# Kernel tuning notes

Measured on AMD Instinct MI355X. Metric: run time of the kernel, lower is better.

The kernel has to match this reference:

```python
import jax, jax.numpy as jnp
import numpy as np

B, IN_F, OUT_F, KD = 256, 1024, 128, 16


def setup_inputs() -> dict:
    key = jax.random.key(0)
    k1, k2 = jax.random.split(key)
    x = jax.random.normal(k1, (B, IN_F), dtype=jnp.float32)
    t_mat = jax.random.normal(k2, (IN_F, OUT_F, KD), dtype=jnp.float32)
    return {"x": x, "t_mat": t_mat}


def reference(x, t_mat):
    # Projection: [B, in] @ [in, out*kd] -> [B, out, kd]
    m = jnp.einsum('bi,iok->bok', x, t_mat)
    # All-pairs L1 distance over kernel dim: [B, B, out]
    norm = jnp.sum(jnp.abs(m[:, None, :, :] - m[None, :, :, :]), axis=-1)
    # exp(-norm) summed over the partner axis; subtract 1 for self-pair (norm=0 -> exp=1)
    o_b = jnp.sum(jnp.exp(-norm), axis=1) - 1.0  # [B, out]
    return jnp.concatenate([x, o_b], axis=1)  # [B, in + out]
```

## Files before the change

### kernel.cpp

```cpp
#include <hip/hip_runtime.h>
#include <hip/hip_fp16.h>


#define BATCH 256
#define INF   1024
#define OUTF  128
#define KDIM  16
#define TCOLS 2048
#define OCOLS 1152
#define XB    1032

typedef __attribute__((ext_vector_type(8))) short short8;
typedef __attribute__((ext_vector_type(4))) float f32x4;

__device__ inline unsigned pack_bf2(float lo, float hi) {
    return __builtin_amdgcn_perm(__float_as_uint(hi), __float_as_uint(lo), 0x07060302u);
}
__device__ inline unsigned short bf_trunc(float f) {
    return (unsigned short)(__float_as_uint(f) >> 16);
}

__global__ __launch_bounds__(256, 2) void k_gemm(const float* __restrict__ x,
                                                 const float* __restrict__ T,
                                                 __half* __restrict__ mh) {
    const int blk = blockIdx.x;
    const int o   = blk & 127;
    const int mq  = blk >> 7;
    const int tid = threadIdx.x;
    const int wave = tid >> 6, lane = tid & 63;
    const int l15 = lane & 15, q = lane >> 4;

    __shared__ unsigned short bs[16][XB];
    __shared__ __half pmout[64][16];

    {
        const int kb = tid >> 2, n0 = (tid & 3) * 4;
        #pragma unroll
        for (int pass = 0; pass < 16; ++pass) {
            const int k = pass * 64 + kb;
            float4 v = *reinterpret_cast<const float4*>(&T[k * TCOLS + o * KDIM + n0]);
            bs[n0 + 0][k] = bf_trunc(v.x);
            bs[n0 + 1][k] = bf_trunc(v.y);
            bs[n0 + 2][k] = bf_trunc(v.z);
            bs[n0 + 3][k] = bf_trunc(v.w);
        }
    }
    __syncthreads();

    const int mt = mq * 4 + wave;
    const float* xr = &x[(mt * 16 + l15) * INF + q * 8];

    float4 st[4][2];
    #pragma unroll
    for (int p = 0; p < 4; ++p) {
        st[p][0] = *reinterpret_cast<const float4*>(xr + p * 32);
        st[p][1] = *reinterpret_cast<const float4*>(xr + p * 32 + 4);
    }
    f32x4 acc = {0.f, 0.f, 0.f, 0.f};
    #pragma unroll
    for (int ks = 0; ks < 32; ++ks) {
        const int p = ks & 3;
        float4 a0 = st[p][0], a1 = st[p][1];
        const int kn = (ks + 4 < 32) ? ks + 4 : ks;
        st[p][0] = *reinterpret_cast<const float4*>(xr + kn * 32);
        st[p][1] = *reinterpret_cast<const float4*>(xr + kn * 32 + 4);
        short8 bfr = *reinterpret_cast<const short8*>(&bs[l15][ks * 32 + q * 8]);
        union { unsigned u[4]; short8 s; } ua;
        ua.u[0] = pack_bf2(a0.x, a0.y); ua.u[1] = pack_bf2(a0.z, a0.w);
        ua.u[2] = pack_bf2(a1.x, a1.y); ua.u[3] = pack_bf2(a1.z, a1.w);
        acc = __builtin_amdgcn_mfma_f32_16x16x32_bf16(ua.s, bfr, acc, 0, 0, 0);
    }

    #pragma unroll
    for (int r = 0; r < 4; ++r)
        pmout[wave * 16 + q * 4 + r][l15] = __float2half(acc[r]);
    __syncthreads();

    if (tid < 128) {
        const int row = tid >> 1, hh = tid & 1;
        uint4 v = *reinterpret_cast<const uint4*>(&pmout[row][hh * 8]);
        *reinterpret_cast<uint4*>(&mh[o * (BATCH * KDIM) + (mq * 64 + row) * KDIM + hh * 8]) = v;
    }
}

__global__ __launch_bounds__(1024) void k_pair(const float* __restrict__ x,
                                               const __half* __restrict__ mh,
                                               float* __restrict__ out) {
    const int blk = blockIdx.x;
    const int o   = blk & 127;
    const int h   = blk >> 7;
    const int tid = threadIdx.x;

    __shared__ __half2 pm[BATCH][8];
    __shared__ float part[32][128];

    if (tid < 256)
        reinterpret_cast<float4*>(out)[blk * 288 + tid] =
            reinterpret_cast<const float4*>(x)[blk * 256 + tid];

    if (tid < 512) {
        uint4 v = *reinterpret_cast<const uint4*>(
            &mh[o * (BATCH * KDIM) + (tid >> 1) * KDIM + (tid & 1) * 8]);
        *reinterpret_cast<uint4*>(&pm[tid >> 1][(tid & 1) * 4]) = v;
    }
    __syncthreads();

    const int i1 = tid & 31;
    const int bsel = tid >> 5;
    __half2 my[4][8];
    #pragma unroll
    for (int r = 0; r < 4; ++r) {
        union { uint4 u[2]; __half2 hh[8]; } c;
        c.u[0] = *reinterpret_cast<const uint4*>(&pm[h * 128 + r * 32 + i1][0]);
        c.u[1] = *reinterpret_cast<const uint4*>(&pm[h * 128 + r * 32 + i1][4]);
        #pragma unroll
        for (int j = 0; j < 8; ++j) my[r][j] = c.hh[j];
    }

    float tot[4] = {0.f, 0.f, 0.f, 0.f};
    const int b2_lo = bsel * 8;
    #pragma unroll
    for (int b2 = b2_lo; b2 < b2_lo + 8; ++b2) {
        union { uint4 u[2]; __half2 hh[8]; } co;
        co.u[0] = *reinterpret_cast<const uint4*>(&pm[b2][0]);
        co.u[1] = *reinterpret_cast<const uint4*>(&pm[b2][4]);
        #pragma unroll
        for (int r = 0; r < 4; ++r) {
            __half2 e0 = __habs2(__hsub2(my[r][0], co.hh[0]));
            __half2 e1 = __habs2(__hsub2(my[r][1], co.hh[1]));
            __half2 e2 = __habs2(__hsub2(my[r][2], co.hh[2]));
            __half2 e3 = __habs2(__hsub2(my[r][3], co.hh[3]));
            e0 = __hadd2(e0, __habs2(__hsub2(my[r][4], co.hh[4])));
            e1 = __hadd2(e1, __habs2(__hsub2(my[r][5], co.hh[5])));
            e2 = __hadd2(e2, __habs2(__hsub2(my[r][6], co.hh[6])));
            e3 = __hadd2(e3, __habs2(__hsub2(my[r][7], co.hh[7])));
            __half2 es = __hadd2(__hadd2(e0, e1), __hadd2(e2, e3));
            float n = __low2float(es) + __high2float(es);
            tot[r] += __expf(-n);
        }
    }
    #pragma unroll
    for (int r = 0; r < 4; ++r)
        part[bsel][r * 32 + i1] = tot[r];
    __syncthreads();

    if (tid < 128) {
        float s = -1.0f;
        #pragma unroll
        for (int j = 0; j < 32; ++j) s += part[j][tid];
        out[(h * 128 + tid) * OCOLS + INF + o] = s;
    }
}

extern "C" void kernel_launch(void* const* d_in, const int* in_sizes, int n_in,
                              void* d_out, int out_size, void* d_ws, size_t ws_size,
                              hipStream_t stream) {
    const float* x = (const float*)d_in[0];
    const float* T = (const float*)d_in[1];
    float* out = (float*)d_out;
    __half* mh = (__half*)d_ws;

    k_gemm<<<512, 256, 0, stream>>>(x, T, mh);
    k_pair<<<256, 1024, 0, stream>>>(x, mh, out);
}
```

Before: 87.89 us.

## Add bf16 prep kernel and rewrite L1 via min identity with exp2

Adds a prep kernel that converts x to bf16 and transposes T to bf16 once, so the GEMM kernel reads MFMA operands straight from global memory with no LDS staging or per-block conversion. The pair kernel rewrites |a-b| as a+b-2*min(a,b), precomputing each row's sum and using packed f16 min plus a single fma and exp2 per pair. This removes the abs/sub ops and T re-reading across blocks, at the cost of an extra launch, extra workspace traffic, and possible fp16 cancellation error in the min-based identity.

```diff
diff --git a/kernel.cpp b/kernel.cpp
--- a/kernel.cpp
+++ b/kernel.cpp
@@ -8,21 +8,75 @@
 #define KDIM  16
 #define TCOLS 2048
 #define OCOLS 1152
-#define XB    1032
 
 typedef __attribute__((ext_vector_type(8))) short short8;
 typedef __attribute__((ext_vector_type(4))) float f32x4;
 
+__device__ inline unsigned short bf_trunc(float f) {
+    return (unsigned short)(__float_as_uint(f) >> 16);
+}
 __device__ inline unsigned pack_bf2(float lo, float hi) {
     return __builtin_amdgcn_perm(__float_as_uint(hi), __float_as_uint(lo), 0x07060302u);
 }
-__device__ inline unsigned short bf_trunc(float f) {
-    return (unsigned short)(__float_as_uint(f) >> 16);
-}
-
-__global__ __launch_bounds__(256, 2) void k_gemm(const float* __restrict__ x,
-                                                 const float* __restrict__ T,
-                                                 __half* __restrict__ mh) {
+__device__ inline __half2 hmin2(__half2 a, __half2 b) {
+    unsigned ua = *reinterpret_cast<unsigned*>(&a);
+    unsigned ub = *reinterpret_cast<unsigned*>(&b);
+    unsigned ud;
+    asm("v_pk_min_f16 %0, %1, %2" : "=v"(ud) : "v"(ua), "v"(ub));
+    return *reinterpret_cast<__half2*>(&ud);
+}
+
+#define TPAD 66
+__global__ __launch_bounds__(256) void k_prep(const float* __restrict__ x,
+                                              const float* __restrict__ T,
+                                              unsigned short* __restrict__ xb,
+                                              unsigned short* __restrict__ tt) {
+    __shared__ unsigned short sm[64][TPAD];
+    const int blk = blockIdx.x, tid = threadIdx.x;
+    if (blk < 512) {
+        const int k0 = (blk & 15) * 64, n0 = (blk >> 4) * 64;
+        {
+            const int r = tid >> 2, cg = (tid & 3) * 16;
+            const float* src = &T[(k0 + r) * TCOLS + n0 + cg];
+            #pragma unroll
+            for (int u = 0; u < 4; ++u) {
+                float4 v = *reinterpret_cast<const float4*>(src + u * 4);
+                sm[r][cg + u*4 + 0] = bf_trunc(v.x);
+                sm[r][cg + u*4 + 1] = bf_trunc(v.y);
+                sm[r][cg + u*4 + 2] = bf_trunc(v.z);
+                sm[r][cg + u*4 + 3] = bf_trunc(v.w);
+            }
+        }
+        __syncthreads();
+        {
+            const int n = tid >> 2, kg = (tid & 3) * 16;
+            unsigned int pk[8];
+            #pragma unroll
+            for (int j = 0; j < 8; ++j)
+                pk[j] = (unsigned int)sm[kg + 2*j][n] |
+                        ((unsigned int)sm[kg + 2*j + 1][n] << 16);
+            uint4* dst = reinterpret_cast<uint4*>(&tt[(n0 + n) * INF + k0 + kg]);
+            dst[0] = make_uint4(pk[0], pk[1], pk[2], pk[3]);
+            dst[1] = make_uint4(pk[4], pk[5], pk[6], pk[7]);
+        }
+    } else {
+        const int base = (blk - 512) * 4096 + tid * 16;
+        unsigned int pk[8];
+        #pragma unroll
+        for (int u = 0; u < 4; ++u) {
+            float4 v = *reinterpret_cast<const float4*>(&x[base + u * 4]);
+            pk[u*2]   = pack_bf2(v.x, v.y);
+            pk[u*2+1] = pack_bf2(v.z, v.w);
+        }
+        uint4* dst = reinterpret_cast<uint4*>(&xb[base]);
+        dst[0] = make_uint4(pk[0], pk[1], pk[2], pk[3]);
+        dst[1] = make_uint4(pk[4], pk[5], pk[6], pk[7]);
+    }
+}
+
+__global__ __launch_bounds__(256) void k_gemm(const unsigned short* __restrict__ xb,
+                                              const unsigned short* __restrict__ tt,
+                                              __half* __restrict__ mh) {
     const int blk = blockIdx.x;
     const int o   = blk & 127;
     const int mq  = blk >> 7;
@@ -30,45 +84,18 @@
     const int wave = tid >> 6, lane = tid & 63;
     const int l15 = lane & 15, q = lane >> 4;
 
-    __shared__ unsigned short bs[16][XB];
     __shared__ __half pmout[64][16];
 
-    {
-        const int kb = tid >> 2, n0 = (tid & 3) * 4;
-        #pragma unroll
-        for (int pass = 0; pass < 16; ++pass) {
-            const int k = pass * 64 + kb;
-            float4 v = *reinterpret_cast<const float4*>(&T[k * TCOLS + o * KDIM + n0]);
-            bs[n0 + 0][k] = bf_trunc(v.x);
-            bs[n0 + 1][k] = bf_trunc(v.y);
-            bs[n0 + 2][k] = bf_trunc(v.z);
-            bs[n0 + 3][k] = bf_trunc(v.w);
-        }
-    }
-    __syncthreads();
-
     const int mt = mq * 4 + wave;
-    const float* xr = &x[(mt * 16 + l15) * INF + q * 8];
-
-    float4 st[4][2];
-    #pragma unroll
-    for (int p = 0; p < 4; ++p) {
-        st[p][0] = *reinterpret_cast<const float4*>(xr + p * 32);
-        st[p][1] = *reinterpret_cast<const float4*>(xr + p * 32 + 4);
-    }
+    const short8* ap = reinterpret_cast<const short8*>(&xb[(mt * 16 + l15) * INF + q * 8]);
+    const short8* bp = reinterpret_cast<const short8*>(&tt[(o * 16 + l15) * INF + q * 8]);
+
     f32x4 acc = {0.f, 0.f, 0.f, 0.f};
-    #pragma unroll
+    #pragma unroll 8
     for (int ks = 0; ks < 32; ++ks) {
-        const int p = ks & 3;
-        float4 a0 = st[p][0], a1 = st[p][1];
-        const int kn = (ks + 4 < 32) ? ks + 4 : ks;
-        st[p][0] = *reinterpret_cast<const float4*>(xr + kn * 32);
-        st[p][1] = *reinterpret_cast<const float4*>(xr + kn * 32 + 4);
-        short8 bfr = *reinterpret_cast<const short8*>(&bs[l15][ks * 32 + q * 8]);
-        union { unsigned u[4]; short8 s; } ua;
-        ua.u[0] = pack_bf2(a0.x, a0.y); ua.u[1] = pack_bf2(a0.z, a0.w);
-        ua.u[2] = pack_bf2(a1.x, a1.y); ua.u[3] = pack_bf2(a1.z, a1.w);
-        acc = __builtin_amdgcn_mfma_f32_16x16x32_bf16(ua.s, bfr, acc, 0, 0, 0);
+        short8 a = ap[ks * 4];
+        short8 b = bp[ks * 4];
+        acc = __builtin_amdgcn_mfma_f32_16x16x32_bf16(a, b, acc, 0, 0, 0);
     }
 
     #pragma unroll
@@ -81,6 +108,22 @@
         uint4 v = *reinterpret_cast<const uint4*>(&pmout[row][hh * 8]);
         *reinterpret_cast<uint4*>(&mh[o * (BATCH * KDIM) + (mq * 64 + row) * KDIM + hh * 8]) = v;
     }
+}
+
+#define L2E  1.4426950408889634f
+#define TL2E 2.8853900817779268f
+
+__device__ inline float ms_chain(const __half2* A, const __half2* B) {
+    __half2 m0 = hmin2(A[0], B[0]);
+    __half2 m1 = hmin2(A[1], B[1]);
+    __half2 m2 = hmin2(A[2], B[2]);
+    __half2 m3 = hmin2(A[3], B[3]);
+    m0 = __hadd2(m0, hmin2(A[4], B[4]));
+    m1 = __hadd2(m1, hmin2(A[5], B[5]));
+    m2 = __hadd2(m2, hmin2(A[6], B[6]));
+    m3 = __hadd2(m3, hmin2(A[7], B[7]));
+    __half2 es = __hadd2(__hadd2(m0, m1), __hadd2(m2, m3));
+    return __low2float(es) + __high2float(es);
 }
 
 __global__ __launch_bounds__(1024) void k_pair(const float* __restrict__ x,
@@ -92,6 +135,7 @@
     const int tid = threadIdx.x;
 
     __shared__ __half2 pm[BATCH][8];
+    __shared__ float Sl2[BATCH];
     __shared__ float part[32][128];
 
     if (tid < 256)
@@ -105,6 +149,13 @@
     }
     __syncthreads();
 
+    if (tid < 256) {
+        union { uint4 u[2]; __half2 hh[8]; } c;
+        c.u[0] = *reinterpret_cast<const uint4*>(&pm[tid][0]);
+        c.u[1] = *reinterpret_cast<const uint4*>(&pm[tid][4]);
+        Sl2[tid] = L2E * ms_chain(c.hh, c.hh);
+    }
+
     const int i1 = tid & 31;
     const int bsel = tid >> 5;
     __half2 my[4][8];
@@ -116,6 +167,11 @@
         #pragma unroll
         for (int j = 0; j < 8; ++j) my[r][j] = c.hh[j];
     }
+    __syncthreads();
+
+    float nsl1[4];
+    #pragma unroll
+    for (int r = 0; r < 4; ++r) nsl1[r] = -Sl2[h * 128 + r * 32 + i1];
 
     float tot[4] = {0.f, 0.f, 0.f, 0.f};
     const int b2_lo = bsel * 8;
@@ -124,19 +180,12 @@
         union { uint4 u[2]; __half2 hh[8]; } co;
         co.u[0] = *reinterpret_cast<const uint4*>(&pm[b2][0]);
         co.u[1] = *reinterpret_cast<const uint4*>(&pm[b2][4]);
+        const float sb2 = Sl2[b2];
         #pragma unroll
         for (int r = 0; r < 4; ++r) {
-            __half2 e0 = __habs2(__hsub2(my[r][0], co.hh[0]));
-            __half2 e1 = __habs2(__hsub2(my[r][1], co.hh[1]));
-            __half2 e2 = __habs2(__hsub2(my[r][2], co.hh[2]));
-            __half2 e3 = __habs2(__hsub2(my[r][3], co.hh[3]));
-            e0 = __hadd2(e0, __habs2(__hsub2(my[r][4], co.hh[4])));
-            e1 = __hadd2(e1, __habs2(__hsub2(my[r][5], co.hh[5])));
-            e2 = __hadd2(e2, __habs2(__hsub2(my[r][6], co.hh[6])));
-            e3 = __hadd2(e3, __habs2(__hsub2(my[r][7], co.hh[7])));
-            __half2 es = __hadd2(__hadd2(e0, e1), __hadd2(e2, e3));
-            float n = __low2float(es) + __high2float(es);
-            tot[r] += __expf(-n);
+            float msf = ms_chain(my[r], co.hh);
+            float arg = fmaf(TL2E, msf, nsl1[r] - sb2);
+            tot[r] += __builtin_amdgcn_exp2f(arg);
         }
     }
     #pragma unroll
@@ -158,8 +207,12 @@
     const float* x = (const float*)d_in[0];
     const float* T = (const float*)d_in[1];
     float* out = (float*)d_out;
-    __half* mh = (__half*)d_ws;
-
-    k_gemm<<<512, 256, 0, stream>>>(x, T, mh);
+
+    unsigned short* xb = (unsigned short*)d_ws;
+    unsigned short* tt = (unsigned short*)((char*)d_ws + (512u << 10));
+    __half*         mh = (__half*)((char*)d_ws + (512u << 10) + (4u << 20));
+
+    k_prep<<<576, 256, 0, stream>>>(x, T, xb, tt);
+    k_gemm<<<512, 256, 0, stream>>>(xb, tt, mh);
     k_pair<<<256, 1024, 0, stream>>>(x, mh, out);
 }
```

Result: no change. 88.21 us (+0.4%).
